# Performance work log

Hardware: AMD Instinct MI355X
Metric: run time of the kernel (lower is better)

Reference implementation:

```python
import jax, jax.numpy as jnp
import numpy as np
from math import sqrt

I = 1024  # input_size
H = 1024  # hidden_size
B = 4096  # batch


def setup_inputs() -> dict:
    key = jax.random.key(0)
    ks = jax.random.split(key, 12)
    a = 1.0 / sqrt(H)
    u = lambda k, shape: jax.random.uniform(k, shape, jnp.float32, -a, a)
    return {
        "x": jax.random.normal(ks[0], (B, I), jnp.float32),
        "hx": jax.random.normal(ks[1], (B, H), jnp.float32),
        "cx": jax.random.normal(ks[2], (B, H), jnp.float32),
        "weight_ih": u(ks[3], (4 * H, I)),
        "weight_hh": u(ks[4], (4 * H, H)),
        "bias_ih": u(ks[5], (4 * H,)),
        "bias_hh": u(ks[6], (4 * H,)),
        "W_peephole_i": u(ks[7], (H, H)),
        "W_peephole_f": u(ks[8], (H, H)),
        "W_peephole_o": u(ks[9], (H, H)),
    }


def reference(x, hx, cx, weight_ih, weight_hh, bias_ih, bias_hh,
              W_peephole_i, W_peephole_f, W_peephole_o):
    # gates: [B, 4H]
    gates = x @ weight_ih.T + bias_ih + hx @ weight_hh.T + bias_hh
    ingate, forgetgate, cellgate, outgate = jnp.split(gates, 4, axis=1)
    # F.linear(cx, W * eye) == cx * diag(W)  (diagonal peephole)
    ingate = jax.nn.sigmoid(ingate + cx * jnp.diagonal(W_peephole_i))
    forgetgate = jax.nn.sigmoid(forgetgate + cx * jnp.diagonal(W_peephole_f))
    cellgate = jnp.tanh(cellgate)
    cy = forgetgate * cx + ingate * cellgate
    # NOTE: original code reuses W_peephole_f for the output gate (faithful to source)
    outgate = jax.nn.sigmoid(outgate + cy * jnp.diagonal(W_peephole_f))
    hy = outgate * jnp.tanh(cy)
    return (hy, cy)
```

## Files before the change

### kernel.cpp

```cpp
#include <hip/hip_runtime.h>
#include <hip/hip_bf16.h>
#include <cstdint>


namespace {

constexpr int H   = 1024;
constexpr int K2  = 2048;
constexpr int BSZ = 4096;
constexpr size_t OUT_CY = (size_t)BSZ * H;

typedef __attribute__((ext_vector_type(8))) short bf16x8;
typedef __attribute__((ext_vector_type(4))) float f32x4;

__device__ __forceinline__ unsigned short f2bf(float f) {
  union { float f; uint32_t u; } v; v.f = f;
  uint32_t u = v.u;
  u += 0x7FFFu + ((u >> 16) & 1u);
  return (unsigned short)(u >> 16);
}

__device__ __forceinline__ float sigm(float x) {
  return 1.0f / (1.0f + __expf(-x));
}
__device__ __forceinline__ float tanh_fast(float x) {
  return 1.0f - 2.0f / (1.0f + __expf(2.0f * x));
}

__device__ __forceinline__ void gload_lds16(const void* g, void* l) {
  __builtin_amdgcn_global_load_lds(
      (const __attribute__((address_space(1))) void*)g,
      (__attribute__((address_space(3))) void*)l, 16, 0, 0);
}

}

__global__ __launch_bounds__(256) void cast_kernel(
    const float* __restrict__ x, const float* __restrict__ hx,
    const float* __restrict__ wih, const float* __restrict__ whh,
    unsigned short* __restrict__ A, unsigned short* __restrict__ W) {
  int b = blockIdx.x;
  bool isW = b >= 8192;
  int t = (isW ? b - 8192 : b) * 256 + threadIdx.x;
  int idx = t * 4;
  int n = idx >> 11;
  int k = idx & 2047;
  const float* s0 = isW ? wih : x;
  const float* s1 = isW ? whh : hx;
  const float* src = (k < H) ? (s0 + (size_t)n * H + k)
                             : (s1 + (size_t)n * H + (k - H));
  float4 v = *(const float4*)src;
  ushort4 o;
  o.x = f2bf(v.x); o.y = f2bf(v.y); o.z = f2bf(v.z); o.w = f2bf(v.w);
  if (isW) {
    int g = n >> 10, h = n & 1023;
    int np = ((h >> 5) << 7) + (g << 5) + (h & 31);
    *(ushort4*)(W + (size_t)np * K2 + k) = o;
  } else {
    *(ushort4*)(A + idx) = o;
  }
}

__global__ __launch_bounds__(128, 2) void lstm_fused_gemm(
    const unsigned short* __restrict__ A,
    const unsigned short* __restrict__ W,
    const float* __restrict__ cx,
    const float* __restrict__ bias_ih, const float* __restrict__ bias_hh,
    const float* __restrict__ Wpi, const float* __restrict__ Wpf,
    float* __restrict__ out) {
  __shared__ __align__(16) unsigned short As[128 * 64];
  __shared__ __align__(16) unsigned short Ws[128 * 64];

  const int tid  = threadIdx.x;
  const int lane = tid & 63;
  const int wave = tid >> 6;
  const int m0 = blockIdx.x * 128;
  const int h0 = blockIdx.y * 32;
  const int w0 = blockIdx.y * 128;

  const int srow = tid >> 3;
  const int scol = (((tid & 7) ^ (srow & 7)) << 3);

  f32x4 acc[4][8];
#pragma unroll
  for (int i = 0; i < 4; ++i)
#pragma unroll
    for (int j = 0; j < 8; ++j)
      acc[i][j] = (f32x4){0.f, 0.f, 0.f, 0.f};

  const int col  = lane & 15;
  const int quad = lane >> 4;
  const int kq   = quad * 8;

  for (int kt = 0; kt < K2 / 64; ++kt) {
    const int kb = kt * 64;
    __syncthreads();
#pragma unroll
    for (int p = 0; p < 8; ++p) {
      const int row = p * 16 + srow;
      const int ldsoff = p * 1024 + wave * 512;
      gload_lds16(A + (size_t)(m0 + row) * K2 + kb + scol, &As[ldsoff]);
      gload_lds16(W + (size_t)(w0 + row) * K2 + kb + scol, &Ws[ldsoff]);
    }
    __syncthreads();

#pragma unroll
    for (int ks = 0; ks < 2; ++ks) {
      const int kk = ks * 32 + kq;
      bf16x8 a[4], b[8];
#pragma unroll
      for (int i = 0; i < 4; ++i) {
        const int R = wave * 64 + i * 16 + col;
        a[i] = *(const bf16x8*)&As[R * 64 + (((kk >> 3) ^ (R & 7)) << 3)];
      }
#pragma unroll
      for (int j = 0; j < 8; ++j) {
        const int R = j * 16 + col;
        b[j] = *(const bf16x8*)&Ws[R * 64 + (((kk >> 3) ^ (R & 7)) << 3)];
      }
#pragma unroll
      for (int i = 0; i < 4; ++i)
#pragma unroll
        for (int j = 0; j < 8; ++j)
          acc[i][j] = __builtin_amdgcn_mfma_f32_16x16x32_bf16(a[i], b[j], acc[i][j], 0, 0, 0);
    }
  }

#pragma unroll
  for (int hh = 0; hh < 2; ++hh) {
    const int h = h0 + hh * 16 + col;
    const float bi = bias_ih[h]         + bias_hh[h];
    const float bf = bias_ih[H + h]     + bias_hh[H + h];
    const float bc = bias_ih[2 * H + h] + bias_hh[2 * H + h];
    const float bo = bias_ih[3 * H + h] + bias_hh[3 * H + h];
    const float di = Wpi[(size_t)h * (H + 1)];
    const float df = Wpf[(size_t)h * (H + 1)];
#pragma unroll
    for (int i = 0; i < 4; ++i) {
#pragma unroll
      for (int r = 0; r < 4; ++r) {
        const int m = m0 + wave * 64 + i * 16 + quad * 4 + r;
        const float c  = cx[(size_t)m * H + h];
        const float ip = acc[i][0 + hh][r] + bi;
        const float fp = acc[i][2 + hh][r] + bf;
        const float cp = acc[i][4 + hh][r] + bc;
        const float op = acc[i][6 + hh][r] + bo;
        const float ig = sigm(ip + c * di);
        const float fg = sigm(fp + c * df);
        const float cg = tanh_fast(cp);
        const float cy = fg * c + ig * cg;
        const float og = sigm(op + cy * df);
        const float hy = og * tanh_fast(cy);
        out[(size_t)m * H + h] = hy;
        out[OUT_CY + (size_t)m * H + h] = cy;
      }
    }
  }
}

extern "C" void kernel_launch(void* const* d_in, const int* in_sizes, int n_in,
                              void* d_out, int out_size, void* d_ws, size_t ws_size,
                              hipStream_t stream) {
  const float* x   = (const float*)d_in[0];
  const float* hx  = (const float*)d_in[1];
  const float* cx  = (const float*)d_in[2];
  const float* wih = (const float*)d_in[3];
  const float* whh = (const float*)d_in[4];
  const float* bih = (const float*)d_in[5];
  const float* bhh = (const float*)d_in[6];
  const float* wpi = (const float*)d_in[7];
  const float* wpf = (const float*)d_in[8];
  float* out = (float*)d_out;

  unsigned short* Abf = (unsigned short*)d_ws;
  unsigned short* Wbf = Abf + (size_t)BSZ * K2;

  cast_kernel<<<16384, 256, 0, stream>>>(x, hx, wih, whh, Abf, Wbf);

  dim3 grid(BSZ / 128, H / 32);
  lstm_fused_gemm<<<grid, 128, 0, stream>>>(Abf, Wbf, cx, bih, bhh, wpi, wpf, out);
}
```

Baseline: 222.9 us.

## Double-buffer LDS tiles with BK=32 to overlap global loads with MFMA

Replaces the single-buffered K=64 loop with a two-stage LDS ping-pong using K=32 tiles. Each iteration issues the next tile's global_load_lds into the alternate buffer, then runs the MFMAs on the current one, with one barrier per iteration instead of two. The swizzle pattern is changed to suit the 32-wide rows. This trades more iterations and smaller tiles for hiding load latency. The async loads are not explicitly waited on before the barrier, so ordering relies on the compiler inserting vmcnt waits.

```diff
diff --git a/kernel.cpp b/kernel.cpp
--- a/kernel.cpp
+++ b/kernel.cpp
@@ -8,6 +8,8 @@
 constexpr int H   = 1024;
 constexpr int K2  = 2048;
 constexpr int BSZ = 4096;
+constexpr int BK  = 32;
+constexpr int NKT = K2 / BK;
 constexpr size_t OUT_CY = (size_t)BSZ * H;
 
 typedef __attribute__((ext_vector_type(8))) short bf16x8;
@@ -68,8 +70,8 @@
     const float* __restrict__ bias_ih, const float* __restrict__ bias_hh,
     const float* __restrict__ Wpi, const float* __restrict__ Wpf,
     float* __restrict__ out) {
-  __shared__ __align__(16) unsigned short As[128 * 64];
-  __shared__ __align__(16) unsigned short Ws[128 * 64];
+  __shared__ __align__(16) unsigned short As[2][128 * BK];
+  __shared__ __align__(16) unsigned short Ws[2][128 * BK];
 
   const int tid  = threadIdx.x;
   const int lane = tid & 63;
@@ -78,8 +80,12 @@
   const int h0 = blockIdx.y * 32;
   const int w0 = blockIdx.y * 128;
 
-  const int srow = tid >> 3;
-  const int scol = (((tid & 7) ^ (srow & 7)) << 3);
+  const int srow4 = tid >> 2;
+  const int cg8   = (((tid & 3) ^ ((tid >> 3) & 3)) << 3);
+
+  const int col  = lane & 15;
+  const int quad = lane >> 4;
+  const int cl8  = ((quad ^ ((col >> 1) & 3)) << 3);
 
   f32x4 acc[4][8];
 #pragma unroll
@@ -88,42 +94,56 @@
     for (int j = 0; j < 8; ++j)
       acc[i][j] = (f32x4){0.f, 0.f, 0.f, 0.f};
 
-  const int col  = lane & 15;
-  const int quad = lane >> 4;
-  const int kq   = quad * 8;
-
-  for (int kt = 0; kt < K2 / 64; ++kt) {
-    const int kb = kt * 64;
-    __syncthreads();
-#pragma unroll
-    for (int p = 0; p < 8; ++p) {
-      const int row = p * 16 + srow;
-      const int ldsoff = p * 1024 + wave * 512;
-      gload_lds16(A + (size_t)(m0 + row) * K2 + kb + scol, &As[ldsoff]);
-      gload_lds16(W + (size_t)(w0 + row) * K2 + kb + scol, &Ws[ldsoff]);
+#pragma unroll
+  for (int p = 0; p < 4; ++p) {
+    const int row = p * 32 + srow4;
+    gload_lds16(A + (size_t)(m0 + row) * K2 + cg8, &As[0][p * 1024 + tid * 8]);
+    gload_lds16(W + (size_t)(w0 + row) * K2 + cg8, &Ws[0][p * 1024 + tid * 8]);
+  }
+  __syncthreads();
+
+  for (int kt = 0; kt < NKT - 1; ++kt) {
+    const int cur = kt & 1;
+    const int nxt = cur ^ 1;
+    const int kbn = (kt + 1) * BK;
+#pragma unroll
+    for (int p = 0; p < 4; ++p) {
+      const int row = p * 32 + srow4;
+      gload_lds16(A + (size_t)(m0 + row) * K2 + kbn + cg8,
+                  &As[nxt][p * 1024 + tid * 8]);
+      gload_lds16(W + (size_t)(w0 + row) * K2 + kbn + cg8,
+                  &Ws[nxt][p * 1024 + tid * 8]);
     }
-    __syncthreads();
-
-#pragma unroll
-    for (int ks = 0; ks < 2; ++ks) {
-      const int kk = ks * 32 + kq;
+    {
       bf16x8 a[4], b[8];
 #pragma unroll
-      for (int i = 0; i < 4; ++i) {
-        const int R = wave * 64 + i * 16 + col;
-        a[i] = *(const bf16x8*)&As[R * 64 + (((kk >> 3) ^ (R & 7)) << 3)];
-      }
-#pragma unroll
-      for (int j = 0; j < 8; ++j) {
-        const int R = j * 16 + col;
-        b[j] = *(const bf16x8*)&Ws[R * 64 + (((kk >> 3) ^ (R & 7)) << 3)];
-      }
+      for (int i = 0; i < 4; ++i)
+        a[i] = *(const bf16x8*)&As[cur][(wave * 64 + i * 16 + col) * BK + cl8];
+#pragma unroll
+      for (int j = 0; j < 8; ++j)
+        b[j] = *(const bf16x8*)&Ws[cur][(j * 16 + col) * BK + cl8];
 #pragma unroll
       for (int i = 0; i < 4; ++i)
 #pragma unroll
         for (int j = 0; j < 8; ++j)
           acc[i][j] = __builtin_amdgcn_mfma_f32_16x16x32_bf16(a[i], b[j], acc[i][j], 0, 0, 0);
     }
+    __syncthreads();
+  }
+  {
+    const int cur = (NKT - 1) & 1;
+    bf16x8 a[4], b[8];
+#pragma unroll
+    for (int i = 0; i < 4; ++i)
+      a[i] = *(const bf16x8*)&As[cur][(wave * 64 + i * 16 + col) * BK + cl8];
+#pragma unroll
+    for (int j = 0; j < 8; ++j)
+      b[j] = *(const bf16x8*)&Ws[cur][(j * 16 + col) * BK + cl8];
+#pragma unroll
+    for (int i = 0; i < 4; ++i)
+#pragma unroll
+      for (int j = 0; j < 8; ++j)
+        acc[i][j] = __builtin_amdgcn_mfma_f32_16x16x32_bf16(a[i], b[j], acc[i][j], 0, 0, 0);
   }
 
 #pragma unroll
```

Result: slower. 247.2 us (+10.9%).

## Double-buffer LDS tiles with BK=32 to overlap global loads with MFMA

Applied to the files above, without the earlier changes.

The K-loop now uses two LDS buffer pairs of 32-wide K tiles instead of a single 64-wide buffer. The next tile is issued via global_load_lds while MFMAs run on the current buffer, with one barrier per tile instead of two. The XOR swizzle is reworked for the 32-element row width. The aim is to hide global-load latency behind compute, at the cost of smaller per-barrier work and a more intricate prologue and epilogue.

```diff
diff --git a/kernel.cpp b/kernel.cpp
--- a/kernel.cpp
+++ b/kernel.cpp
@@ -8,6 +8,8 @@
 constexpr int H   = 1024;
 constexpr int K2  = 2048;
 constexpr int BSZ = 4096;
+constexpr int BK  = 32;
+constexpr int NKT = K2 / BK;
 constexpr size_t OUT_CY = (size_t)BSZ * H;
 
 typedef __attribute__((ext_vector_type(8))) short bf16x8;
@@ -68,8 +70,10 @@
     const float* __restrict__ bias_ih, const float* __restrict__ bias_hh,
     const float* __restrict__ Wpi, const float* __restrict__ Wpf,
     float* __restrict__ out) {
-  __shared__ __align__(16) unsigned short As[128 * 64];
-  __shared__ __align__(16) unsigned short Ws[128 * 64];
+  __shared__ __align__(16) unsigned short As0[128 * BK];
+  __shared__ __align__(16) unsigned short Ws0[128 * BK];
+  __shared__ __align__(16) unsigned short As1[128 * BK];
+  __shared__ __align__(16) unsigned short Ws1[128 * BK];
 
   const int tid  = threadIdx.x;
   const int lane = tid & 63;
@@ -78,8 +82,12 @@
   const int h0 = blockIdx.y * 32;
   const int w0 = blockIdx.y * 128;
 
-  const int srow = tid >> 3;
-  const int scol = (((tid & 7) ^ (srow & 7)) << 3);
+  const int srow4 = tid >> 2;
+  const int cg8   = (((tid & 3) ^ ((tid >> 3) & 3)) << 3);
+
+  const int col  = lane & 15;
+  const int quad = lane >> 4;
+  const int cl8  = ((quad ^ ((col >> 1) & 3)) << 3);
 
   f32x4 acc[4][8];
 #pragma unroll
@@ -88,43 +96,48 @@
     for (int j = 0; j < 8; ++j)
       acc[i][j] = (f32x4){0.f, 0.f, 0.f, 0.f};
 
-  const int col  = lane & 15;
-  const int quad = lane >> 4;
-  const int kq   = quad * 8;
+  auto prefetch = [&](unsigned short (&AS)[128 * BK],
+                      unsigned short (&WS)[128 * BK], int kb) {
+#pragma unroll
+    for (int p = 0; p < 4; ++p) {
+      const int row = p * 32 + srow4;
+      gload_lds16(A + (size_t)(m0 + row) * K2 + kb + cg8, &AS[p * 1024 + tid * 8]);
+      gload_lds16(W + (size_t)(w0 + row) * K2 + kb + cg8, &WS[p * 1024 + tid * 8]);
+    }
+  };
 
-  for (int kt = 0; kt < K2 / 64; ++kt) {
-    const int kb = kt * 64;
+  auto compute = [&](const unsigned short (&AS)[128 * BK],
+                     const unsigned short (&WS)[128 * BK]) {
+    bf16x8 a[4], b[8];
+#pragma unroll
+    for (int i = 0; i < 4; ++i)
+      a[i] = *(const bf16x8*)&AS[(wave * 64 + i * 16 + col) * BK + cl8];
+#pragma unroll
+    for (int j = 0; j < 8; ++j)
+      b[j] = *(const bf16x8*)&WS[(j * 16 + col) * BK + cl8];
+#pragma unroll
+    for (int i = 0; i < 4; ++i)
+#pragma unroll
+      for (int j = 0; j < 8; ++j)
+        acc[i][j] = __builtin_amdgcn_mfma_f32_16x16x32_bf16(a[i], b[j], acc[i][j], 0, 0, 0);
+  };
+
+  prefetch(As0, Ws0, 0);
+  __syncthreads();
+
+  for (int kt2 = 0; kt2 < (NKT - 2) / 2; ++kt2) {
+    const int kb = kt2 * 2 * BK;
+    prefetch(As1, Ws1, kb + BK);
+    compute(As0, Ws0);
     __syncthreads();
-#pragma unroll
-    for (int p = 0; p < 8; ++p) {
-      const int row = p * 16 + srow;
-      const int ldsoff = p * 1024 + wave * 512;
-      gload_lds16(A + (size_t)(m0 + row) * K2 + kb + scol, &As[ldsoff]);
-      gload_lds16(W + (size_t)(w0 + row) * K2 + kb + scol, &Ws[ldsoff]);
-    }
+    prefetch(As0, Ws0, kb + 2 * BK);
+    compute(As1, Ws1);
     __syncthreads();
-
-#pragma unroll
-    for (int ks = 0; ks < 2; ++ks) {
-      const int kk = ks * 32 + kq;
-      bf16x8 a[4], b[8];
-#pragma unroll
-      for (int i = 0; i < 4; ++i) {
-        const int R = wave * 64 + i * 16 + col;
-        a[i] = *(const bf16x8*)&As[R * 64 + (((kk >> 3) ^ (R & 7)) << 3)];
-      }
-#pragma unroll
-      for (int j = 0; j < 8; ++j) {
-        const int R = j * 16 + col;
-        b[j] = *(const bf16x8*)&Ws[R * 64 + (((kk >> 3) ^ (R & 7)) << 3)];
-      }
-#pragma unroll
-      for (int i = 0; i < 4; ++i)
-#pragma unroll
-        for (int j = 0; j < 8; ++j)
-          acc[i][j] = __builtin_amdgcn_mfma_f32_16x16x32_bf16(a[i], b[j], acc[i][j], 0, 0, 0);
-    }
   }
+  prefetch(As1, Ws1, (NKT - 1) * BK);
+  compute(As0, Ws0);
+  __syncthreads();
+  compute(As1, Ws1);
 
 #pragma unroll
   for (int hh = 0; hh < 2; ++hh) {
```

Measured after the change: 231.2 us. +3.7%, slower.
